# Optimization experiments

Measured on AMD Instinct MI355X. Metric: run time of the kernel, lower is better.

## Reference

```python
import jax, jax.numpy as jnp
import numpy as np

SOFT_TAU = 0.5
MAX_TEMP = 40.0
LABEL_SMOOTH = 0.1


def setup_inputs() -> dict:
    key = jax.random.key(0)
    k1, k2 = jax.random.split(key)
    B, Tv, Tw, D = 64, 128, 128, 256
    video_features = jax.random.normal(k1, (B, Tv, D), dtype=jnp.float32)
    wifi_features = jax.random.normal(k2, (B, Tw, D), dtype=jnp.float32)
    logit_scale = jnp.ones((), dtype=jnp.float32)
    return {"video_features": video_features, "wifi_features": wifi_features, "logit_scale": logit_scale}


def _cross_entropy_ls(logits, labels):
    # torch CrossEntropyLoss(label_smoothing=0.1), mean reduction
    logp = jax.nn.log_softmax(logits, axis=-1)
    nll = -jnp.take_along_axis(logp, labels[:, None], axis=1)[:, 0]
    smooth = -jnp.mean(logp, axis=-1)
    return jnp.mean((1.0 - LABEL_SMOOTH) * nll + LABEL_SMOOTH * smooth)


def reference(video_features, wifi_features, logit_scale):
    B = video_features.shape[0]
    # [B, B, Tv, Tw] dense cross-modal similarity
    sim = jnp.einsum('imd,jnd->ijmn', video_features, wifi_features)
    sim_d = jax.lax.stop_gradient(sim)
    # video->wifi soft pooling over Tw
    attn_v2w = jax.nn.softmax(sim_d / SOFT_TAU, axis=3)
    soft_sim_v2w = jnp.sum(sim * attn_v2w, axis=3)  # [B, B, Tv]
    # wifi->video soft pooling over Tv
    attn_w2v = jax.nn.softmax(sim_d / SOFT_TAU, axis=2)
    soft_sim_w2v = jnp.sum(sim * attn_w2v, axis=2)  # [B, B, Tw]
    # frame-level softmax pooling to global similarity
    fw_v = jax.nn.softmax(jax.lax.stop_gradient(soft_sim_v2w) / SOFT_TAU, axis=2)
    sim_v2w_global = jnp.sum(soft_sim_v2w * fw_v, axis=2)  # [B, B]
    fw_w = jax.nn.softmax(jax.lax.stop_gradient(soft_sim_w2v) / SOFT_TAU, axis=2)
    sim_w2v_global = jnp.sum(soft_sim_w2v * fw_w, axis=2)  # [B, B]
    dense_similarity = (sim_v2w_global + sim_w2v_global) / 2.0
    scale = jnp.minimum(logit_scale, MAX_TEMP)
    logits_per_video = scale * dense_similarity
    logits_per_wifi = logits_per_video.T
    labels = jnp.arange(B, dtype=jnp.int32)
    loss_video = _cross_entropy_ls(logits_per_video, labels)
    loss_wifi = _cross_entropy_ls(logits_per_wifi, labels)
    return (loss_video + loss_wifi) / 2.0
```

## Files before the change

kernel.cpp:

```cpp
#include <hip/hip_runtime.h>
#include <hip/hip_bf16.h>

typedef __attribute__((ext_vector_type(8))) short bf16x8;
typedef __attribute__((ext_vector_type(16))) float f32x16;
typedef __attribute__((ext_vector_type(4))) unsigned short u16x4;

#define TT 128
#define DD 256
#define APAN 0
#define BPAN 32768
#define PARTOFF 65536
#define K2L 2.8853900817779268f

__device__ __forceinline__ unsigned short f2bf(float f) {
  unsigned int x = __float_as_uint(f);
  x += 0x7fffu + ((x >> 16) & 1u);
  return (unsigned short)(x >> 16);
}

__device__ __forceinline__ bf16x8 pack8(float4 lo, float4 hi) {
  bf16x8 v;
  v[0] = (short)f2bf(lo.x); v[1] = (short)f2bf(lo.y);
  v[2] = (short)f2bf(lo.z); v[3] = (short)f2bf(lo.w);
  v[4] = (short)f2bf(hi.x); v[5] = (short)f2bf(hi.y);
  v[6] = (short)f2bf(hi.z); v[7] = (short)f2bf(hi.w);
  return v;
}

__global__ __launch_bounds__(256) void conv_kernel(
    const float* __restrict__ v, const float* __restrict__ w,
    unsigned short* __restrict__ vb, unsigned short* __restrict__ wb) {
  const int idx = blockIdx.x * 256 + threadIdx.x;
  float4 a = reinterpret_cast<const float4*>(v)[idx];
  float4 b = reinterpret_cast<const float4*>(w)[idx];
  u16x4 pa, pb;
  pa[0] = f2bf(a.x); pa[1] = f2bf(a.y); pa[2] = f2bf(a.z); pa[3] = f2bf(a.w);
  pb[0] = f2bf(b.x); pb[1] = f2bf(b.y); pb[2] = f2bf(b.z); pb[3] = f2bf(b.w);
  reinterpret_cast<u16x4*>(vb)[idx] = pa;
  reinterpret_cast<u16x4*>(wb)[idx] = pb;
}

#define FR(PAN, ROW, KSLOT)                                                   \
  (*(const bf16x8*)(lds + (PAN) + (ROW) * 256 +                               \
                    ((((KSLOT)) ^ ((ROW) & 15)) << 4)))

template <bool PRE>
__global__ __launch_bounds__(512, 2) void pair_kernel(
    const float* __restrict__ videof, const float* __restrict__ wifif,
    const unsigned short* __restrict__ videob,
    const unsigned short* __restrict__ wifib,
    float* __restrict__ dense) {
  __shared__ __align__(16) char lds[71696];
  const int tid = threadIdx.x;
  const int bid = blockIdx.x;
  const int bi = bid >> 6, bj = bid & 63;
  const int wid = tid >> 6, l = tid & 63;
  const int l31 = l & 31;
  const int khalf = l >> 5;

  const int o  = wid >> 2;
  const int mg = wid & 1;
  const int cg = (wid >> 1) & 1;

  const char* vsrc = (const char*)videob + (size_t)bi * (TT * DD * 2);
  const char* wsrc = (const char*)wifib  + (size_t)bj * (TT * DD * 2);
  const float* vsrcf = videof + (size_t)bi * (TT * DD);
  const float* wsrcf = wifif  + (size_t)bj * (TT * DD);

  const int crow  = l >> 4;
  const int cslot = l & 15;
  const int frow = tid >> 2, fq = tid & 3;

  f32x16 acc[2][2];
#pragma unroll
  for (int mi = 0; mi < 2; ++mi)
#pragma unroll
    for (int t = 0; t < 2; ++t)
#pragma unroll
      for (int r = 0; r < 16; ++r) acc[mi][t][r] = 0.f;

  const int xpan = o ? BPAN : APAN;
  const int ypan = o ? APAN : BPAN;
  const int xr0 = mg * 64 + l31, xr1 = mg * 64 + 32 + l31;
  const int yc0 = cg * 64 + l31, yc1 = cg * 64 + 32 + l31;

#define STAGE_PRE_(KH)                                                        \
  do {                                                                        \
    _Pragma("unroll") for (int k_ = 0; k_ < 8; ++k_) {                        \
      const int q_ = wid * 8 + k_;                                            \
      const int c_ = q_ & 31;                                                 \
      const int r_ = c_ * 4 + crow;                                           \
      const char* s_ = ((q_ < 32) ? vsrc : wsrc) + r_ * 512 + (KH) * 256 +    \
                       ((cslot ^ (r_ & 15)) << 4);                            \
      char* d_ = lds + ((q_ < 32) ? APAN : BPAN) + c_ * 1024;                 \
      __builtin_amdgcn_global_load_lds((const void*)s_, (void*)d_, 16, 0, 0); \
    }                                                                         \
  } while (0)

#define STAGE_REG_(KH)                                                        \
  do {                                                                        \
    _Pragma("unroll") for (int s_ = 0; s_ < 4; ++s_) {                        \
      const int slot_ = fq * 4 + s_;                                          \
      const float* pa_ = vsrcf + frow * DD + (KH) * 128 + slot_ * 8;          \
      const float* pb_ = wsrcf + frow * DD + (KH) * 128 + slot_ * 8;          \
      float4 a0_ = *(const float4*)(pa_);                                     \
      float4 a1_ = *(const float4*)(pa_ + 4);                                 \
      float4 b0_ = *(const float4*)(pb_);                                     \
      float4 b1_ = *(const float4*)(pb_ + 4);                                 \
      const int off_ = frow * 256 + ((slot_ ^ (frow & 15)) << 4);             \
      *(bf16x8*)(lds + APAN + off_) = pack8(a0_, a1_);                        \
      *(bf16x8*)(lds + BPAN + off_) = pack8(b0_, b1_);                        \
    }                                                                         \
  } while (0)

#define COMPUTE_()                                                            \
  do {                                                                        \
    _Pragma("unroll") for (int ksl = 0; ksl < 8; ++ksl) {                     \
      const int kslot_ = 2 * ksl + khalf;                                     \
      bf16x8 x0_ = FR(xpan, xr0, kslot_);                                     \
      bf16x8 x1_ = FR(xpan, xr1, kslot_);                                     \
      bf16x8 y0_ = FR(ypan, yc0, kslot_);                                     \
      bf16x8 y1_ = FR(ypan, yc1, kslot_);                                     \
      acc[0][0] = __builtin_amdgcn_mfma_f32_32x32x16_bf16(x0_, y0_, acc[0][0], 0, 0, 0); \
      acc[0][1] = __builtin_amdgcn_mfma_f32_32x32x16_bf16(x0_, y1_, acc[0][1], 0, 0, 0); \
      acc[1][0] = __builtin_amdgcn_mfma_f32_32x32x16_bf16(x1_, y0_, acc[1][0], 0, 0, 0); \
      acc[1][1] = __builtin_amdgcn_mfma_f32_32x32x16_bf16(x1_, y1_, acc[1][1], 0, 0, 0); \
    }                                                                         \
  } while (0)

  if constexpr (PRE) STAGE_PRE_(0); else STAGE_REG_(0);
  __syncthreads();
  COMPUTE_();
  __syncthreads();
  if constexpr (PRE) STAGE_PRE_(1); else STAGE_REG_(1);
  __syncthreads();
  COMPUTE_();

  float* PM = (float*)(lds + PARTOFF);
  float* PS = PM + 512;
  float* PV = PM + 1024;
  float* Gb = PM + 1536;

#pragma unroll
  for (int t = 0; t < 2; ++t) {
    float mx = acc[0][t][0];
#pragma unroll
    for (int r = 1; r < 16; ++r) mx = fmaxf(mx, acc[0][t][r]);
#pragma unroll
    for (int r = 0; r < 16; ++r) mx = fmaxf(mx, acc[1][t][r]);
    const float mxk = mx * K2L;
    float se = 0.f, sv = 0.f;
#pragma unroll
    for (int mi = 0; mi < 2; ++mi)
#pragma unroll
      for (int r = 0; r < 16; ++r) {
        const float v = acc[mi][t][r];
        const float e = exp2f(fmaf(v, K2L, -mxk));
        se += e;
        sv = fmaf(e, v, sv);
      }
    const float om = __shfl_xor(mx, 32);
    const float os = __shfl_xor(se, 32);
    const float ov = __shfl_xor(sv, 32);
    const float M  = fmaxf(mx, om);
    const float f1 = exp2f((mx - M) * K2L);
    const float f2 = exp2f((om - M) * K2L);
    se = fmaf(se, f1, os * f2);
    sv = fmaf(sv, f1, ov * f2);
    if (l < 32) {
      const int idx = o * 256 + mg * 128 + cg * 64 + t * 32 + l;
      PM[idx] = M; PS[idx] = se; PV[idx] = sv;
    }
  }
  __syncthreads();

  if (tid < 256) {
    const int o2 = tid >> 7, c = tid & 127;
    const int i0 = o2 * 256 + c, i1 = i0 + 128;
    const float m0 = PM[i0], m1 = PM[i1];
    const float M  = fmaxf(m0, m1);
    const float f0 = exp2f((m0 - M) * K2L);
    const float f1 = exp2f((m1 - M) * K2L);
    const float s  = fmaf(PS[i0], f0, PS[i1] * f1);
    const float v  = fmaf(PV[i0], f0, PV[i1] * f1);
    PM[i0] = v / s;
  }
  __syncthreads();

  if (wid < 2) {
    const int oo = (wid == 0) ? 1 : 0;
    float a0 = PM[oo * 256 + l], a1 = PM[oo * 256 + 64 + l];
    float mx = fmaxf(a0, a1);
#pragma unroll
    for (int s = 1; s < 64; s <<= 1) mx = fmaxf(mx, __shfl_xor(mx, s));
    float e0 = exp2f((a0 - mx) * K2L), e1 = exp2f((a1 - mx) * K2L);
    float se = e0 + e1, sev = fmaf(e0, a0, e1 * a1);
#pragma unroll
    for (int s = 1; s < 64; s <<= 1) { se += __shfl_xor(se, s); sev += __shfl_xor(sev, s); }
    if (l == 0) Gb[wid] = sev / se;
  }
  __syncthreads();
  if (tid == 0) dense[bid] = 0.5f * (Gb[0] + Gb[1]);
}

__global__ __launch_bounds__(64) void loss_kernel(
    const float* __restrict__ dense, const float* __restrict__ scalep,
    float* __restrict__ out) {
  const int i = threadIdx.x;
  const float sc = fminf(scalep[0], 40.0f);
  float mxr = -3.4e38f, mxc = -3.4e38f;
  for (int j = 0; j < 64; ++j) {
    mxr = fmaxf(mxr, sc * dense[i * 64 + j]);
    mxc = fmaxf(mxc, sc * dense[j * 64 + i]);
  }
  float ser = 0.f, sec = 0.f, slr = 0.f, slc = 0.f;
  for (int j = 0; j < 64; ++j) {
    float zr = sc * dense[i * 64 + j];
    float zc = sc * dense[j * 64 + i];
    ser += __expf(zr - mxr); sec += __expf(zc - mxc);
    slr += zr;               slc += zc;
  }
  const float lser = mxr + logf(ser);
  const float lsec = mxc + logf(sec);
  const float zd = sc * dense[i * 65];
  float lv = lser - 0.9f * zd - 0.1f * (slr * (1.0f / 64.0f));
  float lw = lsec - 0.9f * zd - 0.1f * (slc * (1.0f / 64.0f));
  float t = 0.5f * (lv + lw);
#pragma unroll
  for (int s = 1; s < 64; s <<= 1) t += __shfl_xor(t, s);
  if (i == 0) out[0] = t * (1.0f / 64.0f);
}

extern "C" void kernel_launch(void* const* d_in, const int* in_sizes, int n_in,
                              void* d_out, int out_size, void* d_ws, size_t ws_size,
                              hipStream_t stream) {
  (void)in_sizes; (void)n_in; (void)out_size;
  const float* video = (const float*)d_in[0];
  const float* wifi  = (const float*)d_in[1];
  const float* scale = (const float*)d_in[2];
  float* dense = (float*)d_ws;
  unsigned short* vb = (unsigned short*)((char*)d_ws + 16384);
  unsigned short* wb = vb + 64 * TT * DD;

  const bool pre = ws_size >= (size_t)16384 + 2u * 64 * TT * DD * 2;
  if (pre) {
    hipLaunchKernelGGL(conv_kernel, dim3(2048), dim3(256), 0, stream,
                       video, wifi, vb, wb);
    hipLaunchKernelGGL((pair_kernel<true>), dim3(64 * 64), dim3(512), 0, stream,
                       video, wifi, vb, wb, dense);
  } else {
    hipLaunchKernelGGL((pair_kernel<false>), dim3(64 * 64), dim3(512), 0, stream,
                       video, wifi, vb, wb, dense);
  }
  hipLaunchKernelGGL(loss_kernel, dim3(1), dim3(64), 0, stream,
                     dense, scale, (float*)d_out);
}
```

Baseline: 108.9 us.

## Double-buffer K tiles with register prefetch and new LDS swizzle layout

Replaces the two-phase (K halves of 128) staging with four K=64 tiles double-buffered in LDS. Each tile's global loads go into registers before the current tile's MFMAs and are written to the other buffer afterwards. This overlaps memory latency with compute and cuts the syncs per tile. The PRE path drops the async global_load_lds in favour of register staging, and a new XOR swizzle with split 8-byte LDS reads and writes is added, which may raise the LDS instruction count.

```diff
diff --git a/kernel.cpp b/kernel.cpp
--- a/kernel.cpp
+++ b/kernel.cpp
@@ -4,13 +4,18 @@
 typedef __attribute__((ext_vector_type(8))) short bf16x8;
 typedef __attribute__((ext_vector_type(16))) float f32x16;
 typedef __attribute__((ext_vector_type(4))) unsigned short u16x4;
+typedef __attribute__((ext_vector_type(2))) unsigned long long u64x2;
 
 #define TT 128
 #define DD 256
-#define APAN 0
-#define BPAN 32768
-#define PARTOFF 65536
+#define BK 64
+#define BPAN 16384
+#define PART 65536
 #define K2L 2.8853900817779268f
+
+__device__ __forceinline__ int poff(int r, int s) {
+  return ((r >> 1) << 8) + ((((s + ((r & 1) << 4)) ^ (r & 31))) << 3);
+}
 
 __device__ __forceinline__ unsigned short f2bf(float f) {
   unsigned int x = __float_as_uint(f);
@@ -39,10 +44,6 @@
   reinterpret_cast<u16x4*>(vb)[idx] = pa;
   reinterpret_cast<u16x4*>(wb)[idx] = pb;
 }
-
-#define FR(PAN, ROW, KSLOT)                                                   \
-  (*(const bf16x8*)(lds + (PAN) + (ROW) * 256 +                               \
-                    ((((KSLOT)) ^ ((ROW) & 15)) << 4)))
 
 template <bool PRE>
 __global__ __launch_bounds__(512, 2) void pair_kernel(
@@ -62,14 +63,12 @@
   const int mg = wid & 1;
   const int cg = (wid >> 1) & 1;
 
-  const char* vsrc = (const char*)videob + (size_t)bi * (TT * DD * 2);
-  const char* wsrc = (const char*)wifib  + (size_t)bj * (TT * DD * 2);
-  const float* vsrcf = videof + (size_t)bi * (TT * DD);
-  const float* wsrcf = wifif  + (size_t)bj * (TT * DD);
-
-  const int crow  = l >> 4;
-  const int cslot = l & 15;
-  const int frow = tid >> 2, fq = tid & 3;
+  const int srow = tid >> 2;
+  const int sq   = tid & 3;
+  const int so0  = poff(srow, sq * 4 + 0);
+  const int so1  = poff(srow, sq * 4 + 1);
+  const int so2  = poff(srow, sq * 4 + 2);
+  const int so3  = poff(srow, sq * 4 + 3);
 
   f32x16 acc[2][2];
 #pragma unroll
@@ -79,48 +78,72 @@
 #pragma unroll
       for (int r = 0; r < 16; ++r) acc[mi][t][r] = 0.f;
 
-  const int xpan = o ? BPAN : APAN;
-  const int ypan = o ? APAN : BPAN;
-  const int xr0 = mg * 64 + l31, xr1 = mg * 64 + 32 + l31;
-  const int yc0 = cg * 64 + l31, yc1 = cg * 64 + 32 + l31;
-
-#define STAGE_PRE_(KH)                                                        \
+  const int xpan = o ? BPAN : 0;
+  const int ypan = o ? 0 : BPAN;
+  const int RX0 = mg * 64 + l31, RX1 = RX0 + 32;
+  const int RY0 = cg * 64 + l31, RY1 = RY0 + 32;
+  const int PBX0 = (RX0 >> 1) << 8, PBX1 = (RX1 >> 1) << 8;
+  const int PBY0 = (RY0 >> 1) << 8, PBY1 = (RY1 >> 1) << 8;
+  const int KLX0 = (((RX0 & 1) << 4) ^ (RX0 & 31)) ^ (khalf << 1);
+  const int KLX1 = (((RX1 & 1) << 4) ^ (RX1 & 31)) ^ (khalf << 1);
+  const int KLY0 = (((RY0 & 1) << 4) ^ (RY0 & 31)) ^ (khalf << 1);
+  const int KLY1 = (((RY1 & 1) << 4) ^ (RY1 & 31)) ^ (khalf << 1);
+
+#define RD(BASE, PB, KL, KS)                                                  \
+  ({                                                                          \
+    const char* p_ = (BASE) + (PB);                                           \
+    const int s0_ = (((KS) << 2) ^ (KL)) << 3;                                \
+    u64x2 t_;                                                                 \
+    t_[0] = *(const unsigned long long*)(p_ + s0_);                           \
+    t_[1] = *(const unsigned long long*)(p_ + (s0_ ^ 8));                     \
+    *(bf16x8*)&t_;                                                            \
+  })
+
+#define STAGE_LOAD(KP, A0, A1, B0, B1)                                        \
   do {                                                                        \
-    _Pragma("unroll") for (int k_ = 0; k_ < 8; ++k_) {                        \
-      const int q_ = wid * 8 + k_;                                            \
-      const int c_ = q_ & 31;                                                 \
-      const int r_ = c_ * 4 + crow;                                           \
-      const char* s_ = ((q_ < 32) ? vsrc : wsrc) + r_ * 512 + (KH) * 256 +    \
-                       ((cslot ^ (r_ & 15)) << 4);                            \
-      char* d_ = lds + ((q_ < 32) ? APAN : BPAN) + c_ * 1024;                 \
-      __builtin_amdgcn_global_load_lds((const void*)s_, (void*)d_, 16, 0, 0); \
+    if constexpr (PRE) {                                                      \
+      const unsigned short* pa_ = videob + (size_t)bi * (TT * DD) +           \
+                                  srow * DD + (KP) * BK + sq * 16;            \
+      const unsigned short* pb_ = wifib + (size_t)bj * (TT * DD) +            \
+                                  srow * DD + (KP) * BK + sq * 16;            \
+      A0 = *(const u64x2*)(pa_);  A1 = *(const u64x2*)(pa_ + 8);              \
+      B0 = *(const u64x2*)(pb_);  B1 = *(const u64x2*)(pb_ + 8);              \
+    } else {                                                                  \
+      const float* pa_ = videof + (size_t)bi * (TT * DD) + srow * DD +        \
+                         (KP) * BK + sq * 16;                                 \
+      const float* pb_ = wifif + (size_t)bj * (TT * DD) + srow * DD +         \
+                         (KP) * BK + sq * 16;                                 \
+      bf16x8 ta0_ = pack8(*(const float4*)(pa_), *(const float4*)(pa_ + 4));  \
+      bf16x8 ta1_ = pack8(*(const float4*)(pa_ + 8), *(const float4*)(pa_ + 12)); \
+      bf16x8 tb0_ = pack8(*(const float4*)(pb_), *(const float4*)(pb_ + 4));  \
+      bf16x8 tb1_ = pack8(*(const float4*)(pb_ + 8), *(const float4*)(pb_ + 12)); \
+      A0 = *(u64x2*)&ta0_; A1 = *(u64x2*)&ta1_;                               \
+      B0 = *(u64x2*)&tb0_; B1 = *(u64x2*)&tb1_;                               \
     }                                                                         \
   } while (0)
 
-#define STAGE_REG_(KH)                                                        \
+#define STAGE_WRITE(BUF, A0, A1, B0, B1)                                      \
   do {                                                                        \
-    _Pragma("unroll") for (int s_ = 0; s_ < 4; ++s_) {                        \
-      const int slot_ = fq * 4 + s_;                                          \
-      const float* pa_ = vsrcf + frow * DD + (KH) * 128 + slot_ * 8;          \
-      const float* pb_ = wsrcf + frow * DD + (KH) * 128 + slot_ * 8;          \
-      float4 a0_ = *(const float4*)(pa_);                                     \
-      float4 a1_ = *(const float4*)(pa_ + 4);                                 \
-      float4 b0_ = *(const float4*)(pb_);                                     \
-      float4 b1_ = *(const float4*)(pb_ + 4);                                 \
-      const int off_ = frow * 256 + ((slot_ ^ (frow & 15)) << 4);             \
-      *(bf16x8*)(lds + APAN + off_) = pack8(a0_, a1_);                        \
-      *(bf16x8*)(lds + BPAN + off_) = pack8(b0_, b1_);                        \
-    }                                                                         \
+    char* ba_ = lds + (BUF) * 32768;                                          \
+    *(unsigned long long*)(ba_ + so0) = A0[0];                                \
+    *(unsigned long long*)(ba_ + so1) = A0[1];                                \
+    *(unsigned long long*)(ba_ + so2) = A1[0];                                \
+    *(unsigned long long*)(ba_ + so3) = A1[1];                                \
+    *(unsigned long long*)(ba_ + BPAN + so0) = B0[0];                         \
+    *(unsigned long long*)(ba_ + BPAN + so1) = B0[1];                         \
+    *(unsigned long long*)(ba_ + BPAN + so2) = B1[0];                         \
+    *(unsigned long long*)(ba_ + BPAN + so3) = B1[1];                         \
   } while (0)
 
-#define COMPUTE_()                                                            \
+#define COMPUTE(BUF)                                                          \
   do {                                                                        \
-    _Pragma("unroll") for (int ksl = 0; ksl < 8; ++ksl) {                     \
-      const int kslot_ = 2 * ksl + khalf;                                     \
-      bf16x8 x0_ = FR(xpan, xr0, kslot_);                                     \
-      bf16x8 x1_ = FR(xpan, xr1, kslot_);                                     \
-      bf16x8 y0_ = FR(ypan, yc0, kslot_);                                     \
-      bf16x8 y1_ = FR(ypan, yc1, kslot_);                                     \
+    const char* xb_ = lds + (BUF) * 32768 + xpan;                             \
+    const char* yb_ = lds + (BUF) * 32768 + ypan;                             \
+    _Pragma("unroll") for (int ks = 0; ks < 4; ++ks) {                        \
+      bf16x8 x0_ = RD(xb_, PBX0, KLX0, ks);                                   \
+      bf16x8 x1_ = RD(xb_, PBX1, KLX1, ks);                                   \
+      bf16x8 y0_ = RD(yb_, PBY0, KLY0, ks);                                   \
+      bf16x8 y1_ = RD(yb_, PBY1, KLY1, ks);                                   \
       acc[0][0] = __builtin_amdgcn_mfma_f32_32x32x16_bf16(x0_, y0_, acc[0][0], 0, 0, 0); \
       acc[0][1] = __builtin_amdgcn_mfma_f32_32x32x16_bf16(x0_, y1_, acc[0][1], 0, 0, 0); \
       acc[1][0] = __builtin_amdgcn_mfma_f32_32x32x16_bf16(x1_, y0_, acc[1][0], 0, 0, 0); \
@@ -128,15 +151,23 @@
     }                                                                         \
   } while (0)
 
-  if constexpr (PRE) STAGE_PRE_(0); else STAGE_REG_(0);
-  __syncthreads();
-  COMPUTE_();
-  __syncthreads();
-  if constexpr (PRE) STAGE_PRE_(1); else STAGE_REG_(1);
-  __syncthreads();
-  COMPUTE_();
-
-  float* PM = (float*)(lds + PARTOFF);
+  {
+    u64x2 a0, a1, b0, b1;
+    STAGE_LOAD(0, a0, a1, b0, b1);
+    STAGE_WRITE(0, a0, a1, b0, b1);
+  }
+  __syncthreads();
+
+#pragma unroll
+  for (int kp = 0; kp < 4; ++kp) {
+    u64x2 a0, a1, b0, b1;
+    if (kp < 3) STAGE_LOAD(kp + 1, a0, a1, b0, b1);
+    COMPUTE(kp & 1);
+    if (kp < 3) STAGE_WRITE((kp + 1) & 1, a0, a1, b0, b1);
+    __syncthreads();
+  }
+
+  float* PM = (float*)(lds + PART);
   float* PS = PM + 512;
   float* PV = PM + 1024;
   float* Gb = PM + 1536;
@@ -188,8 +219,8 @@
   __syncthreads();
 
   if (wid < 2) {
-    const int oo = (wid == 0) ? 1 : 0;
-    float a0 = PM[oo * 256 + l], a1 = PM[oo * 256 + 64 + l];
+    const float* RS = PM + (wid == 0 ? 256 : 0);
+    float a0 = RS[l], a1 = RS[64 + l];
     float mx = fmaxf(a0, a1);
 #pragma unroll
     for (int s = 1; s < 64; s <<= 1) mx = fmaxf(mx, __shfl_xor(mx, s));
```

Measured after the change: 106.3 us. 1.02x faster.
